# Kernel tuning notes

Hardware: AMD Instinct MI355X
Metric: run time of the kernel (lower is better)

## Reference

```python
import jax, jax.numpy as jnp
import numpy as np

V, E, H = 128, 256, 1024
B, T = 128, 512

def setup_inputs() -> dict:
    key = jax.random.key(0)
    ks = jax.random.split(key, 7)
    tokens = jax.random.randint(ks[0], (B, T), 0, V)
    emb = jax.random.normal(ks[1], (V, E), jnp.float32) * 0.05
    W = jax.random.normal(ks[2], (E, 4 * H), jnp.float32) * (1.0 / np.sqrt(E))
    U = jax.random.normal(ks[3], (H, 4 * H), jnp.float32) * (1.0 / np.sqrt(H))
    b = jnp.zeros((4 * H,), jnp.float32)
    Wd = jax.random.normal(ks[4], (H, V), jnp.float32) * (1.0 / np.sqrt(H))
    bd = jnp.zeros((V,), jnp.float32)
    return {"tokens": tokens, "emb": emb, "W": W, "U": U, "b": b, "Wd": Wd, "bd": bd}

def _masked_lstm(x, mask, W, U, b):
    # x: [B,T,E], mask: [B,T] bool. Keras semantics: masked steps carry h,c
    # forward unchanged (output at masked step = previous output).
    xz = jnp.einsum('bte,ef->btf', x, W) + b  # precompute input projection [B,T,4H]
    h0 = jnp.zeros((x.shape[0], U.shape[0]), x.dtype)
    c0 = jnp.zeros_like(h0)

    def step(carry, inp):
        h, c = carry
        xz_t, m_t = inp  # [B,4H], [B]
        z = xz_t + h @ U
        i, f, g, o = jnp.split(z, 4, axis=-1)
        i = jax.nn.sigmoid(i)
        f = jax.nn.sigmoid(f)
        g = jnp.tanh(g)
        o = jax.nn.sigmoid(o)
        c_new = f * c + i * g
        h_new = o * jnp.tanh(c_new)
        m = m_t[:, None]
        h_out = jnp.where(m, h_new, h)
        c_out = jnp.where(m, c_new, c)
        return (h_out, c_out), h_out

    (hT, cT), hs = jax.lax.scan(step, (h0, c0),
                                (jnp.swapaxes(xz, 0, 1), jnp.swapaxes(mask, 0, 1)))
    return jnp.swapaxes(hs, 0, 1), hT, cT  # [B,T,H], [B,H], [B,H]

def reference(tokens, emb, W, U, b, Wd, bd):
    x = emb[tokens]                    # [B,T,E] embedding lookup
    mask = tokens != 0                 # [B,T]
    states, h, c = _masked_lstm(x, mask, W, U, b)
    logits = jnp.einsum('bth,hv->btv', states, Wd) + bd
    return jax.nn.softmax(logits, axis=-1)
```

## Files before the change

kernel.cpp:

```cpp
#include <hip/hip_runtime.h>
#include <stdio.h>


typedef _Float16 f16;
typedef f16 f16x8 __attribute__((ext_vector_type(8)));
typedef f16 f16x4 __attribute__((ext_vector_type(4)));
typedef float f32x4 __attribute__((ext_vector_type(4)));
typedef unsigned int u32;
typedef u32 u32x4 __attribute__((ext_vector_type(4)));

static constexpr int V = 128, E = 256, H = 1024, NB = 128, T = 512, FH = 4096;

static constexpr size_t OFF_CTRL = 0;
static constexpr size_t SZ_CTRL  = 16384;
static constexpr size_t OFF_HB0  = SZ_CTRL;
static constexpr size_t SZ_HB    = (size_t)16384 * 16;
static constexpr size_t OFF_HB1  = OFF_HB0 + SZ_HB;
static constexpr size_t OFF_EMBW = OFF_HB1 + SZ_HB;
static constexpr size_t SZ_EMBW  = (size_t)V * FH * 4;
static constexpr size_t OFF_UF   = OFF_EMBW + SZ_EMBW;
static constexpr size_t SZ_UF    = (size_t)H * FH * 2;
static constexpr size_t OFF_WD   = OFF_UF + SZ_UF;
static constexpr size_t SZ_WD    = (size_t)H * V * 2;
static constexpr size_t OFF_ST   = OFF_WD + SZ_WD;
static constexpr size_t SZ_ST    = (size_t)NB * T * H * 2;
static constexpr size_t WS_NEED  = OFF_ST + SZ_ST;

__device__ __forceinline__ float fast_sigmoid(float x) {
  return __builtin_amdgcn_rcpf(1.f + __expf(-x));
}
__device__ __forceinline__ float fast_tanh(float x) {
  const float e = __expf(2.f * x);
  return (e - 1.f) * __builtin_amdgcn_rcpf(e + 1.f);
}

__global__ void prep_embW(const float* __restrict__ emb, const float* __restrict__ W,
                          const float* __restrict__ bias, float* __restrict__ embW) {
  const int j  = blockIdx.x * 16 + (threadIdx.x & 15);
  const int vg = threadIdx.x >> 4;
  float a[8];
  const float bj = bias[j];
#pragma unroll
  for (int r = 0; r < 8; ++r) a[r] = bj;
  for (int e = 0; e < E; ++e) {
    const float wv = W[(size_t)e * FH + j];
#pragma unroll
    for (int r = 0; r < 8; ++r) a[r] += emb[(size_t)(vg * 8 + r) * E + e] * wv;
  }
#pragma unroll
  for (int r = 0; r < 8; ++r) embW[(size_t)(vg * 8 + r) * FH + j] = a[r];
}

__global__ void prep_U(const float* __restrict__ U, f16* __restrict__ uf) {
  const int q  = blockIdx.x * 256 + threadIdx.x;
  const int k  = q >> 9;
  const int j0 = (q & 511) * 8;
  const int w = k >> 7, kk = (k >> 5) & 3, l4s = (k >> 3) & 3, es = k & 7;
  const float* row = U + (size_t)k * FH + j0;
#pragma unroll
  for (int i = 0; i < 8; ++i) {
    const int j = j0 + i;
    const int g2 = j >> 10, r = j & 1023;
    const int cgv = r >> 5, s = r & 31;
    const int nt = g2 * 2 + (s >> 4), l15 = s & 15;
    const int chunk = (((cgv * 8 + w) * 8 + nt) * 4 + kk) * 64 + l4s * 16 + l15;
    uf[(size_t)chunk * 8 + es] = (f16)row[i];
  }
}

__global__ void prep_Wd(const float* __restrict__ Wd, f16* __restrict__ wd) {
  const int c = blockIdx.x * 256 + threadIdx.x;
  const int lane = c & 63, kk = (c >> 6) & 31, nt = c >> 11;
  const int k0 = kk * 32 + ((lane >> 4) << 3);
  const int v  = nt * 16 + (lane & 15);
  f16x8 o;
#pragma unroll
  for (int e = 0; e < 8; ++e) o[e] = (f16)Wd[(size_t)(k0 + e) * V + v];
  ((f16x8*)wd)[c] = o;
}

__global__ __launch_bounds__(512, 2) void lstm_kernel(
    const int*   __restrict__ tok,
    const float* __restrict__ embW,
    const f16x8* __restrict__ Ufrag,
    u32x4* hB0, u32x4* hB1,
    f16* __restrict__ st,
    int* ctrl)
{
  const int blk = blockIdx.x;
  const int tid = threadIdx.x;
  const int w = tid >> 6, lane = tid & 63;
  const int l15 = lane & 15, l4 = lane >> 4;

  int* initctr = ctrl;
  int* xcdcnt  = ctrl + 8;
  int* flags   = ctrl + 1024;

  __shared__ f16 zph[2][8][129][20];
  __shared__ int s_bg, s_cg, s_fast;

  const int myxcd = (int)(__builtin_amdgcn_s_getreg(6164) & 15);
  if (tid == 0) {
    const int rank = __hip_atomic_fetch_add(&xcdcnt[myxcd & 7], 1,
                                            __ATOMIC_RELAXED, __HIP_MEMORY_SCOPE_AGENT);
    __hip_atomic_fetch_add(initctr, 1, __ATOMIC_RELEASE, __HIP_MEMORY_SCOPE_AGENT);
    int spins = 0;
    while (__hip_atomic_load(initctr, __ATOMIC_RELAXED, __HIP_MEMORY_SCOPE_AGENT) < 256) {
      __builtin_amdgcn_s_sleep(8);
      if (++spins > (1 << 15)) break;
    }
    const int total = __hip_atomic_load(initctr, __ATOMIC_ACQUIRE,
                                        __HIP_MEMORY_SCOPE_AGENT);
    int fast = (total >= 256) ? 1 : 0;
    for (int i = 0; i < 8; ++i)
      fast &= (__hip_atomic_load(&xcdcnt[i], __ATOMIC_RELAXED,
                                 __HIP_MEMORY_SCOPE_AGENT) == 32) ? 1 : 0;
    s_fast = fast;
    s_bg = fast ? (myxcd & 7) : (blk & 7);
    s_cg = fast ? rank        : (blk >> 3);
  }
  __syncthreads();
  const int FAST = s_fast;
  const int bg = s_bg, cg = s_cg;

  f16x8 Bf[8][4];
  {
    const f16x8* up = Ufrag + (size_t)(cg * 8 + w) * 2048;
#pragma unroll
    for (int nt = 0; nt < 8; ++nt)
#pragma unroll
      for (int kk = 0; kk < 4; ++kk)
        Bf[nt][kk] = up[(nt * 4 + kk) * 64 + lane];
  }

  const int m_g = tid >> 5;
  const int l_g = tid & 31;
  const int b_g = bg * 16 + m_g;
  const int j_g = cg * 32 + l_g;
  const int w_s = cg >> 2, kk_s = cg & 3, l4_s = l_g >> 3;
  const int pidx = (((bg * 8 + w_s) * 4 + l4_s) * 4 + kk_s) * 16 + m_g;
  int* pflag = flags + ((bg * 8 + w_s) * 4 + kk_s) * 8 + w;
  float c_st = 0.f, h_st = 0.f;

  const int cbase = (((bg * 8 + w) * 4 + l4) * 4) * 16 + l15;
  const int* fpoll = flags + (bg * 8 + w) * 32 + (lane & 31);

  const size_t stbase = (((size_t)(j_g >> 3)) * 16 + m_g) * 8 + (j_g & 7);

  for (int t = 0; t < T; ++t) {
    const int tk = tok[(size_t)b_g * T + t];
    const float* ew = embW + (size_t)tk * FH + j_g;
    const float x0 = ew[0], x1 = ew[1024], x2 = ew[2048], x3 = ew[3072];

    {
      int fv, spins = 0;
      for (;;) {
        asm volatile("global_load_dword %0, %1, off sc0 sc1\n\t"
                     "s_waitcnt vmcnt(0)"
                     : "=v"(fv) : "v"(fpoll) : "memory");
        if (__all(fv >= t)) break;
        if (++spins > (1 << 17)) break;
        if (spins > 512 && (spins & 63) == 0)
          asm volatile("buffer_inv sc1" ::: "memory");
        if (spins > 16) __builtin_amdgcn_s_sleep(1);
      }
    }

    const u32x4* hb = ((t & 1) ? hB1 : hB0) + cbase;
    u32x4 e0, e1, e2, e3;
    asm volatile(
        "global_load_dwordx4 %0, %4, off sc0 sc1\n\t"
        "global_load_dwordx4 %1, %4, off offset:256 sc0 sc1\n\t"
        "global_load_dwordx4 %2, %4, off offset:512 sc0 sc1\n\t"
        "global_load_dwordx4 %3, %4, off offset:768 sc0 sc1\n\t"
        "s_waitcnt vmcnt(0)"
        : "=&v"(e0), "=&v"(e1), "=&v"(e2), "=&v"(e3)
        : "v"(hb)
        : "memory");
    const f16x8 a0 = __builtin_bit_cast(f16x8, e0);
    const f16x8 a1 = __builtin_bit_cast(f16x8, e1);
    const f16x8 a2 = __builtin_bit_cast(f16x8, e2);
    const f16x8 a3 = __builtin_bit_cast(f16x8, e3);

    f32x4 acc[8];
#pragma unroll
    for (int nt = 0; nt < 8; ++nt) acc[nt] = (f32x4){0.f, 0.f, 0.f, 0.f};
#define MF(AH, KK)                                                                 \
  {                                                                                \
    _Pragma("unroll")                                                              \
    for (int nt = 0; nt < 8; ++nt)                                                 \
      acc[nt] = __builtin_amdgcn_mfma_f32_16x16x32_f16(AH, Bf[nt][KK], acc[nt], 0, 0, 0); \
  }
    MF(a0, 0) MF(a1, 1) MF(a2, 2) MF(a3, 3)
#undef MF

    const int par = t & 1;
#pragma unroll
    for (int nt = 0; nt < 8; ++nt) {
      f16x4 v4;
#pragma unroll
      for (int r = 0; r < 4; ++r) v4[r] = (f16)acc[nt][r];
      *(f16x4*)&zph[par][w][nt * 16 + l15][l4 * 4] = v4;
    }
    __syncthreads();

    float z0 = x0, z1 = x1, z2 = x2, z3 = x3;
#pragma unroll
    for (int q = 0; q < 8; ++q) {
      z0 += (float)zph[par][q][l_g][m_g];
      z1 += (float)zph[par][q][32 + l_g][m_g];
      z2 += (float)zph[par][q][64 + l_g][m_g];
      z3 += (float)zph[par][q][96 + l_g][m_g];
    }
    const float ig = fast_sigmoid(z0);
    const float fg = fast_sigmoid(z1);
    const float gg = fast_tanh(z2);
    const float og = fast_sigmoid(z3);
    const float cn = fg * c_st + ig * gg;
    const float hn = og * fast_tanh(cn);
    if (tk != 0) { c_st = cn; h_st = hn; }

    const f16 hv = (f16)h_st;

    const u32 hbits = (u32)__builtin_bit_cast(unsigned short, hv);
    const u32 p  = hbits | ((u32)__shfl_xor((int)hbits, 1, 64) << 16);
    const u32 q2 = (u32)__shfl_xor((int)p, 2, 64);
    const u32 r2 = (u32)__shfl_xor((int)p, 4, 64);
    const u32 s2 = (u32)__shfl_xor((int)q2, 4, 64);
    if ((l_g & 7) == 0) {
      u32x4 val = {p, q2, r2, s2};
      u32x4* dst = ((t & 1) ? hB0 : hB1) + pidx;
      if (FAST)
        asm volatile("global_store_dwordx4 %0, %1, off"
                     :: "v"(dst), "v"(val) : "memory");
      else
        asm volatile("global_store_dwordx4 %0, %1, off sc0 sc1"
                     :: "v"(dst), "v"(val) : "memory");
    }

    asm volatile("s_waitcnt vmcnt(0)" ::: "memory");
    if (lane == 0) {
      const int tv = t + 1;
      if (FAST)
        asm volatile("global_store_dword %0, %1, off"
                     :: "v"(pflag), "v"(tv) : "memory");
      else
        asm volatile("global_store_dword %0, %1, off sc0 sc1"
                     :: "v"(pflag), "v"(tv) : "memory");
    }

    st[(size_t)(t * 8 + bg) * 16384 + stbase] = hv;
  }
}

__global__ __launch_bounds__(512, 2) void logits_kernel(
    const uint4* __restrict__ st, const uint4* __restrict__ wd,
    const float* __restrict__ bd, float* __restrict__ out)
{
  __shared__ f16 As[256 * 64];
  __shared__ f16 Bs[64 * 128];
  const int tid = threadIdx.x;
  const int w = tid >> 6, lane = tid & 63;
  const int l15 = lane & 15, l4 = lane >> 4;
  const int rblk0 = blockIdx.x * 16;

  f32x4 acc[2][8];
#pragma unroll
  for (int rb = 0; rb < 2; ++rb)
#pragma unroll
    for (int nt = 0; nt < 8; ++nt) acc[rb][nt] = (f32x4){0.f, 0.f, 0.f, 0.f};

  for (int ph = 0; ph < 16; ++ph) {
    __syncthreads();
#pragma unroll
    for (int i = 0; i < 4; ++i) {
      const int cc = tid * 4 + i;
      const int rb = cc >> 7, kc = (cc >> 4) & 7, m = cc & 15;
      ((uint4*)As)[cc] = st[((size_t)(rblk0 + rb) * 128 + ph * 8 + kc) * 16 + m];
    }
#pragma unroll
    for (int i = 0; i < 2; ++i) {
      const int cc = tid * 2 + i;
      const int lc = cc & 63, kkl = (cc >> 6) & 1, nt = cc >> 7;
      ((uint4*)Bs)[cc] = wd[((size_t)nt * 32 + ph * 2 + kkl) * 64 + lc];
    }
    __syncthreads();
#pragma unroll
    for (int kkl = 0; kkl < 2; ++kkl)
#pragma unroll
      for (int rb = 0; rb < 2; ++rb) {
        const f16x8 a = ((const f16x8*)As)[((w * 2 + rb) * 8 + kkl * 4 + l4) * 16 + l15];
#pragma unroll
        for (int nt = 0; nt < 8; ++nt)
          acc[rb][nt] = __builtin_amdgcn_mfma_f32_16x16x32_f16(
              a, ((const f16x8*)Bs)[(nt * 2 + kkl) * 64 + lane], acc[rb][nt], 0, 0, 0);
      }
  }

#pragma unroll
  for (int rb = 0; rb < 2; ++rb) {
    float mx[4] = {-3.0e38f, -3.0e38f, -3.0e38f, -3.0e38f};
#pragma unroll
    for (int nt = 0; nt < 8; ++nt) {
      const float bv = bd[nt * 16 + l15];
#pragma unroll
      for (int r = 0; r < 4; ++r) {
        acc[rb][nt][r] += bv;
        mx[r] = fmaxf(mx[r], acc[rb][nt][r]);
      }
    }
#pragma unroll
    for (int d = 1; d < 16; d <<= 1)
#pragma unroll
      for (int r = 0; r < 4; ++r) mx[r] = fmaxf(mx[r], __shfl_xor(mx[r], d, 64));
    float sm[4] = {0.f, 0.f, 0.f, 0.f};
#pragma unroll
    for (int nt = 0; nt < 8; ++nt)
#pragma unroll
      for (int r = 0; r < 4; ++r) {
        const float p = expf(acc[rb][nt][r] - mx[r]);
        acc[rb][nt][r] = p;
        sm[r] += p;
      }
#pragma unroll
    for (int d = 1; d < 16; d <<= 1)
#pragma unroll
      for (int r = 0; r < 4; ++r) sm[r] += __shfl_xor(sm[r], d, 64);
#pragma unroll
    for (int r = 0; r < 4; ++r) {
      const float inv = 1.f / sm[r];
      const int rg = (rblk0 + w * 2 + rb) * 16 + l4 * 4 + r;
      const int bb = rg & 127, tt = rg >> 7;
      float* op = out + ((size_t)bb * T + tt) * V;
#pragma unroll
      for (int nt = 0; nt < 8; ++nt) op[nt * 16 + l15] = acc[rb][nt][r] * inv;
    }
  }
}

extern "C" void kernel_launch(void* const* d_in, const int* in_sizes, int n_in,
                              void* d_out, int out_size, void* d_ws, size_t ws_size,
                              hipStream_t stream) {
  const int*   tokens = (const int*)d_in[0];
  const float* emb    = (const float*)d_in[1];
  const float* W      = (const float*)d_in[2];
  const float* U      = (const float*)d_in[3];
  const float* bias   = (const float*)d_in[4];
  const float* Wd     = (const float*)d_in[5];
  const float* bd     = (const float*)d_in[6];
  float* out = (float*)d_out;
  char* ws = (char*)d_ws;

  if (ws_size < WS_NEED) {
    fprintf(stderr, "kernel_launch: ws too small: %zu < %zu\n", ws_size, WS_NEED);
    return;
  }

  int*   ctrl = (int*)(ws + OFF_CTRL);
  u32x4* hB0  = (u32x4*)(ws + OFF_HB0);
  u32x4* hB1  = (u32x4*)(ws + OFF_HB1);
  float* embW = (float*)(ws + OFF_EMBW);
  f16*   uf   = (f16*)(ws + OFF_UF);
  f16*   wdf  = (f16*)(ws + OFF_WD);
  f16*   st   = (f16*)(ws + OFF_ST);

  (void)hipMemsetAsync(ws, 0, OFF_EMBW, stream);

  prep_embW<<<256, 256, 0, stream>>>(emb, W, bias, embW);
  prep_U<<<2048, 256, 0, stream>>>(U, uf);
  prep_Wd<<<64, 256, 0, stream>>>(Wd, wdf);

  lstm_kernel<<<256, 512, 0, stream>>>(tokens, embW, (const f16x8*)uf,
                                       hB0, hB1, st, ctrl);

  logits_kernel<<<256, 512, 0, stream>>>((const uint4*)st, (const uint4*)wdf,
                                         bd, out);
}
```

Measured before the change: 1.120 ms.

## Repartition recurrent matmul across waves as 4 K-groups by 2 N-groups

Changes how each block's 8 waves split the h@U product: instead of each wave covering a 128-wide K slice across all 8 N tiles, waves are arranged as 4 K-groups by 2 N-groups, each handling a 256-wide K slice over 4 N tiles. The U fragment layout, the hidden-state buffer indexing and the flag layout are all reworked to match. The cross-wave reduction through shared memory shrinks from 8 partials to 4, and each wave now polls 64 flags and loads 8 h fragments per step. The spin loop also drops the periodic cache invalidate and delays the sleep, trading more aggressive polling for lower synchronization latency.

New measurement: 1.063 ms. 5.1% less time.

```diff
diff --git a/kernel.cpp b/kernel.cpp
--- a/kernel.cpp
+++ b/kernel.cpp
@@ -55,16 +55,17 @@
   const int q  = blockIdx.x * 256 + threadIdx.x;
   const int k  = q >> 9;
   const int j0 = (q & 511) * 8;
-  const int w = k >> 7, kk = (k >> 5) & 3, l4s = (k >> 3) & 3, es = k & 7;
+  const int kg = k >> 8, kk = (k >> 5) & 7, l4s = (k >> 3) & 3, es = k & 7;
   const float* row = U + (size_t)k * FH + j0;
 #pragma unroll
   for (int i = 0; i < 8; ++i) {
     const int j = j0 + i;
-    const int g2 = j >> 10, r = j & 1023;
-    const int cgv = r >> 5, s = r & 31;
-    const int nt = g2 * 2 + (s >> 4), l15 = s & 15;
-    const int chunk = (((cgv * 8 + w) * 8 + nt) * 4 + kk) * 64 + l4s * 16 + l15;
-    uf[(size_t)chunk * 8 + es] = (f16)row[i];
+    const int g = j >> 10, cg = (j >> 5) & 31, s = j & 31;
+    const int n = g * 32 + s;
+    const int ng = n >> 6, nt = (n >> 4) & 3, l15 = n & 15;
+    const int w = ng * 4 + kg;
+    const int chunk = ((cg * 8 + w) * 4 + nt) * 8 + kk;
+    uf[((size_t)chunk * 64 + l4s * 16 + l15) * 8 + es] = (f16)row[i];
   }
 }
 
@@ -91,6 +92,7 @@
   const int tid = threadIdx.x;
   const int w = tid >> 6, lane = tid & 63;
   const int l15 = lane & 15, l4 = lane >> 4;
+  const int kg = w & 3, ng = w >> 2;
 
   int* initctr = ctrl;
   int* xcdcnt  = ctrl + 8;
@@ -123,27 +125,27 @@
   const int FAST = s_fast;
   const int bg = s_bg, cg = s_cg;
 
-  f16x8 Bf[8][4];
+  f16x8 Bf[4][8];
   {
     const f16x8* up = Ufrag + (size_t)(cg * 8 + w) * 2048;
 #pragma unroll
-    for (int nt = 0; nt < 8; ++nt)
-#pragma unroll
-      for (int kk = 0; kk < 4; ++kk)
-        Bf[nt][kk] = up[(nt * 4 + kk) * 64 + lane];
+    for (int nt = 0; nt < 4; ++nt)
+#pragma unroll
+      for (int kk = 0; kk < 8; ++kk)
+        Bf[nt][kk] = up[(nt * 8 + kk) * 64 + lane];
   }
 
   const int m_g = tid >> 5;
   const int l_g = tid & 31;
   const int b_g = bg * 16 + m_g;
   const int j_g = cg * 32 + l_g;
-  const int w_s = cg >> 2, kk_s = cg & 3, l4_s = l_g >> 3;
-  const int pidx = (((bg * 8 + w_s) * 4 + l4_s) * 4 + kk_s) * 16 + m_g;
-  int* pflag = flags + ((bg * 8 + w_s) * 4 + kk_s) * 8 + w;
+  const int kg_s = cg >> 3, kk_s = cg & 7, l4_s = l_g >> 3;
+  const int pidx = (((bg * 4 + kg_s) * 4 + l4_s) * 8 + kk_s) * 16 + m_g;
+  int* pflag = flags + (bg * 4 + kg_s) * 64 + kk_s * 8 + w;
   float c_st = 0.f, h_st = 0.f;
 
-  const int cbase = (((bg * 8 + w) * 4 + l4) * 4) * 16 + l15;
-  const int* fpoll = flags + (bg * 8 + w) * 32 + (lane & 31);
+  const int cbase = (((bg * 4 + kg) * 4 + l4) * 8) * 16 + l15;
+  const int* fpoll = flags + (bg * 4 + kg) * 64 + lane;
 
   const size_t stbase = (((size_t)(j_g >> 3)) * 16 + m_g) * 8 + (j_g & 7);
 
@@ -160,53 +162,61 @@
                      : "=v"(fv) : "v"(fpoll) : "memory");
         if (__all(fv >= t)) break;
         if (++spins > (1 << 17)) break;
-        if (spins > 512 && (spins & 63) == 0)
-          asm volatile("buffer_inv sc1" ::: "memory");
-        if (spins > 16) __builtin_amdgcn_s_sleep(1);
+        if (spins > 2048) __builtin_amdgcn_s_sleep(1);
       }
     }
 
     const u32x4* hb = ((t & 1) ? hB1 : hB0) + cbase;
-    u32x4 e0, e1, e2, e3;
+    u32x4 e0, e1, e2, e3, e4, e5, e6, e7;
     asm volatile(
-        "global_load_dwordx4 %0, %4, off sc0 sc1\n\t"
-        "global_load_dwordx4 %1, %4, off offset:256 sc0 sc1\n\t"
-        "global_load_dwordx4 %2, %4, off offset:512 sc0 sc1\n\t"
-        "global_load_dwordx4 %3, %4, off offset:768 sc0 sc1\n\t"
+        "global_load_dwordx4 %0, %8, off sc0 sc1\n\t"
+        "global_load_dwordx4 %1, %8, off offset:256 sc0 sc1\n\t"
+        "global_load_dwordx4 %2, %8, off offset:512 sc0 sc1\n\t"
+        "global_load_dwordx4 %3, %8, off offset:768 sc0 sc1\n\t"
+        "global_load_dwordx4 %4, %8, off offset:1024 sc0 sc1\n\t"
+        "global_load_dwordx4 %5, %8, off offset:1280 sc0 sc1\n\t"
+        "global_load_dwordx4 %6, %8, off offset:1536 sc0 sc1\n\t"
+        "global_load_dwordx4 %7, %8, off offset:1792 sc0 sc1\n\t"
         "s_waitcnt vmcnt(0)"
-        : "=&v"(e0), "=&v"(e1), "=&v"(e2), "=&v"(e3)
+        : "=&v"(e0), "=&v"(e1), "=&v"(e2), "=&v"(e3),
+          "=&v"(e4), "=&v"(e5), "=&v"(e6), "=&v"(e7)
         : "v"(hb)
         : "memory");
     const f16x8 a0 = __builtin_bit_cast(f16x8, e0);
     const f16x8 a1 = __builtin_bit_cast(f16x8, e1);
     const f16x8 a2 = __builtin_bit_cast(f16x8, e2);
     const f16x8 a3 = __builtin_bit_cast(f16x8, e3);
-
-    f32x4 acc[8];
-#pragma unroll
-    for (int nt = 0; nt < 8; ++nt) acc[nt] = (f32x4){0.f, 0.f, 0.f, 0.f};
+    const f16x8 a4 = __builtin_bit_cast(f16x8, e4);
+    const f16x8 a5 = __builtin_bit_cast(f16x8, e5);
+    const f16x8 a6 = __builtin_bit_cast(f16x8, e6);
+    const f16x8 a7 = __builtin_bit_cast(f16x8, e7);
+
+    f32x4 acc[4];
+#pragma unroll
+    for (int nt = 0; nt < 4; ++nt) acc[nt] = (f32x4){0.f, 0.f, 0.f, 0.f};
 #define MF(AH, KK)                                                                 \
   {                                                                                \
     _Pragma("unroll")                                                              \
-    for (int nt = 0; nt < 8; ++nt)                                                 \
+    for (int nt = 0; nt < 4; ++nt)                                                 \
       acc[nt] = __builtin_amdgcn_mfma_f32_16x16x32_f16(AH, Bf[nt][KK], acc[nt], 0, 0, 0); \
   }
     MF(a0, 0) MF(a1, 1) MF(a2, 2) MF(a3, 3)
+    MF(a4, 4) MF(a5, 5) MF(a6, 6) MF(a7, 7)
 #undef MF
 
     const int par = t & 1;
 #pragma unroll
-    for (int nt = 0; nt < 8; ++nt) {
+    for (int nt = 0; nt < 4; ++nt) {
       f16x4 v4;
 #pragma unroll
       for (int r = 0; r < 4; ++r) v4[r] = (f16)acc[nt][r];
-      *(f16x4*)&zph[par][w][nt * 16 + l15][l4 * 4] = v4;
+      *(f16x4*)&zph[par][kg][ng * 64 + nt * 16 + l15][l4 * 4] = v4;
     }
     __syncthreads();
 
     float z0 = x0, z1 = x1, z2 = x2, z3 = x3;
 #pragma unroll
-    for (int q = 0; q < 8; ++q) {
+    for (int q = 0; q < 4; ++q) {
       z0 += (float)zph[par][q][l_g][m_g];
       z1 += (float)zph[par][q][32 + l_g][m_g];
       z2 += (float)zph[par][q][64 + l_g][m_g];
```
